# Optimization experiments

Measured on AMD Instinct MI355X. Metric: run time of the kernel, lower is better.

Reference implementation:

```python
import jax, jax.numpy as jnp
import numpy as np

N = 100000
E = 3200000
D = 128


def setup_inputs() -> dict:
    key = jax.random.key(0)
    k1, k2, k3, k4 = jax.random.split(key, 4)
    x = jax.random.normal(k1, (N, D), dtype=jnp.float32)
    edge_index = jax.random.randint(k2, (2, E), 0, N, dtype=jnp.int64)
    W1 = jax.random.normal(k3, (D, 16), dtype=jnp.float32) * (1.0 / np.sqrt(D))
    b1 = jnp.zeros((16,), dtype=jnp.float32)
    W2 = jax.random.normal(k4, (16, 2), dtype=jnp.float32) * (1.0 / np.sqrt(16))
    b2 = jnp.zeros((2,), dtype=jnp.float32)
    return {"x": x, "edge_index": edge_index, "W1": W1, "b1": b1, "W2": W2, "b2": b2}


def _gcn_conv(h, src, dst, norm, W, b):
    # transform first (out_dim <= in_dim), then normalized scatter-add aggregation
    h = h @ W                                   # [N, out]
    msg = h[src] * norm[:, None]                # [E+N, out] gathered messages
    agg = jax.ops.segment_sum(msg, dst, num_segments=N)
    return agg + b


def reference(x, edge_index, W1, b1, W2, b2):
    loops = jnp.arange(N, dtype=edge_index.dtype)
    src = jnp.concatenate([edge_index[0], loops])   # row (message source)
    dst = jnp.concatenate([edge_index[1], loops])   # col (aggregation target)
    # symmetric GCN normalization: deg over dst, norm = d^-1/2[src] * d^-1/2[dst]
    deg = jax.ops.segment_sum(jnp.ones_like(src, dtype=x.dtype), dst, num_segments=N)
    dinv = jnp.where(deg > 0, jax.lax.rsqrt(deg), 0.0)
    norm = dinv[src] * dinv[dst]

    h = _gcn_conv(x, src, dst, norm, W1, b1)
    h = jax.nn.relu(h)
    h = _gcn_conv(h, src, dst, norm, W2, b2)
    return jax.nn.log_softmax(h, axis=1)
```

## Files before the change

### kernel.cpp

```cpp
#include <hip/hip_runtime.h>
#include <hip/hip_fp16.h>
#include <math.h>

#define N_NODES 100000
#define N_EDGES 3200000
#define D_IN    128
#define H1      16

#define PSH     8
#define NPB     200
#define NB      500
#define CAP     9936
#define PBLK    512
#define CHUNK   6250
#define ELS_CAP 13760
#define NLINES  (ELS_CAP / 16)
#define MROWS   64

__device__ __forceinline__ unsigned bkt(int d) {
    return (unsigned)(((unsigned long long)(unsigned)d * 671089ull) >> 27);
}


__global__ __launch_bounds__(512) void k_partition(const int* __restrict__ ei,
                                                   int* __restrict__ cursor,
                                                   unsigned int* __restrict__ eop) {
    __shared__ int h[512];
    __shared__ int loff[512];
    __shared__ int resv[NB];
    __shared__ int wsum[8], wpre[8];
    __shared__ unsigned short owner[NLINES];
    __shared__ unsigned char rank8[CHUNK];
    __shared__ unsigned int els[ELS_CAP];
    int t = threadIdx.x;
    h[t] = 0;
    __syncthreads();
    int c0 = blockIdx.x * CHUNK;
    const int2* s2 = (const int2*)(ei + c0);
    const int2* d2 = (const int2*)(ei + N_EDGES + c0);
    for (int i = t; i < CHUNK / 2; i += 512) {
        int2 dd = d2[i];
        rank8[2 * i]     = (unsigned char)atomicAdd(&h[bkt(dd.x)], 1);
        rank8[2 * i + 1] = (unsigned char)atomicAdd(&h[bkt(dd.y)], 1);
    }
    __syncthreads();
    int cp = (h[t] + 15) & ~15;
    int lane = t & 63, w = t >> 6;
    int v = cp;
#pragma unroll
    for (int o = 1; o < 64; o <<= 1) {
        int u = __shfl_up(v, o);
        if (lane >= o) v += u;
    }
    if (lane == 63) wsum[w] = v;
    __syncthreads();
    if (t < 8) {
        int s = wsum[t];
#pragma unroll
        for (int o = 1; o < 8; o <<= 1) {
            int u = __shfl_up(s, o);
            if (t >= o) s += u;
        }
        wpre[t] = s;
    }
    __syncthreads();
    int inc = v + ((w > 0) ? wpre[w - 1] : 0);
    int totalpad = wpre[7];
    int ex = inc - cp;
    loff[t] = ex;
    if (t < NB && cp) {
        resv[t] = atomicAdd(&cursor[t], cp);
        int l0 = ex >> 4;
        for (int k = 0; k < (cp >> 4); ++k) owner[l0 + k] = (unsigned short)t;
    }
    for (int i = t; i < totalpad; i += 512) els[i] = 0xFFFFFFFFu;
    __syncthreads();
    for (int i = t; i < CHUNK / 2; i += 512) {
        int2 ss = s2[i];
        int2 dd = d2[i];
        unsigned bx = bkt(dd.x), by = bkt(dd.y);
        els[loff[bx] + (int)rank8[2 * i]] =
            ((unsigned)ss.x << PSH) | (unsigned)(dd.x - (int)(bx * NPB));
        els[loff[by] + (int)rank8[2 * i + 1]] =
            ((unsigned)ss.y << PSH) | (unsigned)(dd.y - (int)(by * NPB));
    }
    __syncthreads();
    for (int i = t; i < totalpad; i += 512) {
        int b   = owner[i >> 4];
        int pos = resv[b] + (i - loff[b]);
        if (pos < CAP)
            eop[(size_t)b * CAP + pos] = els[i];
    }
}

__global__ __launch_bounds__(512) void k_build(const int* __restrict__ cursor,
                                               unsigned int* __restrict__ eop,
                                               int* __restrict__ nstart,
                                               int* __restrict__ ndeg,
                                               float* __restrict__ dinv) {
    __shared__ unsigned int els[CAP];
    __shared__ int cnt[256];
    __shared__ int off[256];
    __shared__ int wsum[4], wpre[4];
    int t = threadIdx.x, b = blockIdx.x;
    if (t < 256) cnt[t] = 0;
    __syncthreads();
    int n = cursor[b]; if (n > CAP) n = CAP;
    unsigned int* reg = eop + (size_t)b * CAP;
    for (int i4 = t; i4 < (n >> 2); i4 += 512) {
        uint4 wv = ((const uint4*)reg)[i4];
        unsigned int e0 = wv.x, e1 = wv.y, e2 = wv.z, e3 = wv.w;
        int r;
        if ((int)e0 >= 0) { r = atomicAdd(&cnt[e0 & 0xFF], 1); e0 |= (unsigned)r << 25; }
        if ((int)e1 >= 0) { r = atomicAdd(&cnt[e1 & 0xFF], 1); e1 |= (unsigned)r << 25; }
        if ((int)e2 >= 0) { r = atomicAdd(&cnt[e2 & 0xFF], 1); e2 |= (unsigned)r << 25; }
        if ((int)e3 >= 0) { r = atomicAdd(&cnt[e3 & 0xFF], 1); e3 |= (unsigned)r << 25; }
        ((uint4*)els)[i4] = make_uint4(e0, e1, e2, e3);
    }
    __syncthreads();
    int lane = t & 63, w = t >> 6;
    int v = 0;
    if (t < 256) {
        v = cnt[t];
#pragma unroll
        for (int o = 1; o < 64; o <<= 1) {
            int u = __shfl_up(v, o);
            if (lane >= o) v += u;
        }
        if (lane == 63) wsum[w] = v;
    }
    __syncthreads();
    if (t < 4) {
        int s = wsum[t];
#pragma unroll
        for (int o = 1; o < 4; o <<= 1) {
            int u = __shfl_up(s, o);
            if (t >= o) s += u;
        }
        wpre[t] = s;
    }
    __syncthreads();
    if (t < 256) {
        int val = cnt[t];
        int ex = (v + ((w > 0) ? wpre[w - 1] : 0)) - val;
        off[t] = ex;
        if (t < NPB) {
            int node = b * NPB + t;
            nstart[node] = b * CAP + ex;
            ndeg[node]   = val;
            dinv[node]   = rsqrtf((float)(val + 1));
        }
    }
    __syncthreads();
    for (int i4 = t; i4 < (n >> 2); i4 += 512) {
        uint4 wv = ((const uint4*)els)[i4];
        unsigned int e; unsigned s;
        e = wv.x; s = (e >> PSH) & 0x1FFFFu;
        if (s < N_NODES) reg[off[e & 0xFF] + (int)(e >> 25)] = s;
        e = wv.y; s = (e >> PSH) & 0x1FFFFu;
        if (s < N_NODES) reg[off[e & 0xFF] + (int)(e >> 25)] = s;
        e = wv.z; s = (e >> PSH) & 0x1FFFFu;
        if (s < N_NODES) reg[off[e & 0xFF] + (int)(e >> 25)] = s;
        e = wv.w; s = (e >> PSH) & 0x1FFFFu;
        if (s < N_NODES) reg[off[e & 0xFF] + (int)(e >> 25)] = s;
    }
}

__global__ __launch_bounds__(256) void k_mm1(const float* __restrict__ x,
                                             const float* __restrict__ W1,
                                             const float* __restrict__ dinv,
                                             __half* __restrict__ h1h) {
    __shared__ float sX[MROWS][D_IN + 1];
    int t = threadIdx.x;
    int r0 = blockIdx.x * MROWS;
    for (int i = t; i < MROWS * (D_IN / 4); i += 256) {
        int row = i >> 5, c4 = i & 31;
        int grow = r0 + row;
        float4 v = (grow < N_NODES) ? ((const float4*)x)[(size_t)grow * 32 + c4]
                                    : make_float4(0.f, 0.f, 0.f, 0.f);
        sX[row][c4 * 4 + 0] = v.x; sX[row][c4 * 4 + 1] = v.y;
        sX[row][c4 * 4 + 2] = v.z; sX[row][c4 * 4 + 3] = v.w;
    }
    __syncthreads();
    int lane = t & 63;
    int c0 = __builtin_amdgcn_readfirstlane((t >> 6) * 4);
    float a0 = 0.f, a1 = 0.f, a2 = 0.f, a3 = 0.f;
#pragma unroll 4
    for (int d = 0; d < D_IN; ++d) {
        float xv = sX[lane][d];
        a0 = fmaf(xv, W1[d * 16 + c0 + 0], a0);
        a1 = fmaf(xv, W1[d * 16 + c0 + 1], a1);
        a2 = fmaf(xv, W1[d * 16 + c0 + 2], a2);
        a3 = fmaf(xv, W1[d * 16 + c0 + 3], a3);
    }
    int grow = r0 + lane;
    if (grow < N_NODES) {
        float di = dinv[grow];
        __half2* o = (__half2*)(h1h + (size_t)grow * H1 + c0);
        o[0] = __floats2half2_rn(a0 * di, a1 * di);
        o[1] = __floats2half2_rn(a2 * di, a3 * di);
    }
}

__global__ __launch_bounds__(256) void k_agg1(const unsigned int* __restrict__ eop,
                                              const int* __restrict__ nstart,
                                              const int* __restrict__ ndeg,
                                              const __half* __restrict__ h1h,
                                              const float* __restrict__ dinv,
                                              const float* __restrict__ b1,
                                              const float* __restrict__ W2,
                                              float2* __restrict__ h2f) {
    int t = threadIdx.x;
    int g = t >> 3, l = t & 7;
    int base = (t & 63) & ~7;
    int node = blockIdx.x * 32 + g;
    int e0 = nstart[node], deg = ndeg[node];
    const __half2* H = (const __half2*)h1h;
    float a0 = 0.f, a1 = 0.f, c0 = 0.f, c1 = 0.f;
    int nfull = deg & ~7;
    int j = e0;
    for (; j < e0 + nfull; j += 8) {
        int s = (int)eop[j + l];
#pragma unroll
        for (int k = 0; k < 8; k += 2) {
            int sk0 = __shfl(s, base + k);
            int sk1 = __shfl(s, base + k + 1);
            float2 f0 = __half22float2(H[sk0 * 8 + l]);
            float2 f1 = __half22float2(H[sk1 * 8 + l]);
            a0 += f0.x; a1 += f0.y;
            c0 += f1.x; c1 += f1.y;
        }
    }
    int r = e0 + deg - j;
    if (r) {
        int s = (l < r) ? (int)eop[j + l] : -1;
#pragma unroll
        for (int k = 0; k < 8; ++k) {
            int sk = __shfl(s, base + k);
            int su = (sk >= 0) ? sk : 0;
            float m = (sk >= 0) ? 1.f : 0.f;
            float2 f = __half22float2(H[su * 8 + l]);
            a0 = fmaf(f.x, m, a0); a1 = fmaf(f.y, m, a1);
        }
    }
    float di = dinv[node];
    float2 self = __half22float2(H[node * 8 + l]);
    float s0 = (a0 + c0) + self.x, s1 = (a1 + c1) + self.y;
    float2 bb = ((const float2*)b1)[l];
    float h0 = fmaxf(fmaf(di, s0, bb.x), 0.f);
    float h1v = fmaxf(fmaf(di, s1, bb.y), 0.f);
    float4 wv = ((const float4*)W2)[l];
    float p0 = h0 * wv.x + h1v * wv.z;
    float p1 = h0 * wv.y + h1v * wv.w;
#pragma unroll
    for (int off = 1; off < 8; off <<= 1) {
        p0 += __shfl_xor(p0, off);
        p1 += __shfl_xor(p1, off);
    }
    if (l == 0) h2f[node] = make_float2(p0 * di, p1 * di);
}

__global__ __launch_bounds__(256) void k_agg2(const unsigned int* __restrict__ eop,
                                              const int* __restrict__ nstart,
                                              const int* __restrict__ ndeg,
                                              const float2* __restrict__ h2f,
                                              const float* __restrict__ dinv,
                                              const float* __restrict__ b2,
                                              float* __restrict__ out) {
    int tg = blockIdx.x * 256 + threadIdx.x;
    int node = tg >> 2, l = tg & 3;
    if (node >= N_NODES) return;
    int e0 = nstart[node], e1 = e0 + ndeg[node];
    float ax = 0.f, ay = 0.f;
    for (int j = e0 + l; j < e1; j += 4) {
        float2 m = h2f[eop[j]];
        ax += m.x; ay += m.y;
    }
    ax += __shfl_xor(ax, 1); ay += __shfl_xor(ay, 1);
    ax += __shfl_xor(ax, 2); ay += __shfl_xor(ay, 2);
    if (l == 0) {
        float di = dinv[node];
        float2 self = h2f[node];
        float a0 = fmaf(di, ax + self.x, b2[0]);
        float a1 = fmaf(di, ay + self.y, b2[1]);
        float m  = fmaxf(a0, a1);
        float lg = logf(expf(a0 - m) + expf(a1 - m));
        out[2 * node]     = a0 - m - lg;
        out[2 * node + 1] = a1 - m - lg;
    }
}

extern "C" void kernel_launch(void* const* d_in, const int* in_sizes, int n_in,
                              void* d_out, int out_size, void* d_ws, size_t ws_size,
                              hipStream_t stream) {
    const float* x  = (const float*)d_in[0];
    const int*   ei = (const int*)d_in[1];
    const float* W1 = (const float*)d_in[2];
    const float* b1 = (const float*)d_in[3];
    const float* W2 = (const float*)d_in[4];
    const float* b2 = (const float*)d_in[5];
    float* out = (float*)d_out;

    int*          cursor = (int*)d_ws;
    int*          nstart = cursor + 512;
    int*          ndeg   = nstart + 100352;
    float*        dinv   = (float*)(ndeg + 100352);
    __half*       h1h    = (__half*)(dinv + 100352);
    float2*       h2f    = (float2*)(h1h + (size_t)100352 * H1);
    unsigned int* eop    = (unsigned int*)(h2f + 100352);

    hipMemsetAsync(cursor, 0, 512 * sizeof(int), stream);
    k_partition<<<PBLK, 512, 0, stream>>>(ei, cursor, eop);
    k_build    <<<NB,   512, 0, stream>>>(cursor, eop, nstart, ndeg, dinv);
    k_mm1      <<<(N_NODES + MROWS - 1) / MROWS, 256, 0, stream>>>(x, W1, dinv, h1h);
    k_agg1     <<<N_NODES / 32, 256, 0, stream>>>(eop, nstart, ndeg, h1h, dinv, b1, W2, h2f);
    k_agg2     <<<(N_NODES * 4 + 255) / 256, 256, 0, stream>>>(eop, nstart, ndeg, h2f, dinv, b2, out);
}
```

Before: 204.0 us.

## Scatter partitioned edges directly to global, pad cursors, widen agg2 lanes

The partition kernel no longer stages edges in a large shared-memory buffer with prefix sums and an owner table. It now writes each edge straight to its global bucket slot and pads each reservation with sentinel values. Per-bucket cursors are spaced 32 ints apart so the atomics on them do not contend within a cache line. The second aggregation uses 8 lanes per node instead of 4. Dropping the large LDS buffer should raise occupancy, at the cost of scattered, uncoalesced global writes.

Measured after the change: 221.7 us. 8.7% more time.

```diff
diff --git a/kernel.cpp b/kernel.cpp
--- a/kernel.cpp
+++ b/kernel.cpp
@@ -13,8 +13,7 @@
 #define CAP     9936
 #define PBLK    512
 #define CHUNK   6250
-#define ELS_CAP 13760
-#define NLINES  (ELS_CAP / 16)
+#define CSTRIDE 32
 #define MROWS   64
 
 __device__ __forceinline__ unsigned bkt(int d) {
@@ -26,12 +25,8 @@
                                                    int* __restrict__ cursor,
                                                    unsigned int* __restrict__ eop) {
     __shared__ int h[512];
-    __shared__ int loff[512];
     __shared__ int resv[NB];
-    __shared__ int wsum[8], wpre[8];
-    __shared__ unsigned short owner[NLINES];
     __shared__ unsigned char rank8[CHUNK];
-    __shared__ unsigned int els[ELS_CAP];
     int t = threadIdx.x;
     h[t] = 0;
     __syncthreads();
@@ -44,52 +39,30 @@
         rank8[2 * i + 1] = (unsigned char)atomicAdd(&h[bkt(dd.y)], 1);
     }
     __syncthreads();
-    int cp = (h[t] + 15) & ~15;
-    int lane = t & 63, w = t >> 6;
-    int v = cp;
-#pragma unroll
-    for (int o = 1; o < 64; o <<= 1) {
-        int u = __shfl_up(v, o);
-        if (lane >= o) v += u;
-    }
-    if (lane == 63) wsum[w] = v;
-    __syncthreads();
-    if (t < 8) {
-        int s = wsum[t];
-#pragma unroll
-        for (int o = 1; o < 8; o <<= 1) {
-            int u = __shfl_up(s, o);
-            if (t >= o) s += u;
-        }
-        wpre[t] = s;
-    }
-    __syncthreads();
-    int inc = v + ((w > 0) ? wpre[w - 1] : 0);
-    int totalpad = wpre[7];
-    int ex = inc - cp;
-    loff[t] = ex;
-    if (t < NB && cp) {
-        resv[t] = atomicAdd(&cursor[t], cp);
-        int l0 = ex >> 4;
-        for (int k = 0; k < (cp >> 4); ++k) owner[l0 + k] = (unsigned short)t;
-    }
-    for (int i = t; i < totalpad; i += 512) els[i] = 0xFFFFFFFFu;
+    if (t < NB) {
+        int cnt = h[t];
+        int cp  = (cnt + 15) & ~15;
+        int rv  = cp ? atomicAdd(&cursor[t * CSTRIDE], cp) : 0;
+        resv[t] = rv;
+        unsigned int* regb = eop + (size_t)t * CAP;
+        for (int i = cnt; i < cp; ++i) {
+            int pos = rv + i;
+            if (pos < CAP) regb[pos] = 0xFFFFFFFFu;
+        }
+    }
     __syncthreads();
     for (int i = t; i < CHUNK / 2; i += 512) {
         int2 ss = s2[i];
         int2 dd = d2[i];
         unsigned bx = bkt(dd.x), by = bkt(dd.y);
-        els[loff[bx] + (int)rank8[2 * i]] =
-            ((unsigned)ss.x << PSH) | (unsigned)(dd.x - (int)(bx * NPB));
-        els[loff[by] + (int)rank8[2 * i + 1]] =
-            ((unsigned)ss.y << PSH) | (unsigned)(dd.y - (int)(by * NPB));
-    }
-    __syncthreads();
-    for (int i = t; i < totalpad; i += 512) {
-        int b   = owner[i >> 4];
-        int pos = resv[b] + (i - loff[b]);
-        if (pos < CAP)
-            eop[(size_t)b * CAP + pos] = els[i];
+        int px = resv[bx] + (int)rank8[2 * i];
+        int py = resv[by] + (int)rank8[2 * i + 1];
+        if (px < CAP)
+            eop[(size_t)bx * CAP + px] =
+                ((unsigned)ss.x << PSH) | (unsigned)(dd.x - (int)(bx * NPB));
+        if (py < CAP)
+            eop[(size_t)by * CAP + py] =
+                ((unsigned)ss.y << PSH) | (unsigned)(dd.y - (int)(by * NPB));
     }
 }
 
@@ -105,7 +78,7 @@
     int t = threadIdx.x, b = blockIdx.x;
     if (t < 256) cnt[t] = 0;
     __syncthreads();
-    int n = cursor[b]; if (n > CAP) n = CAP;
+    int n = cursor[b * CSTRIDE]; if (n > CAP) n = CAP;
     unsigned int* reg = eop + (size_t)b * CAP;
     for (int i4 = t; i4 < (n >> 2); i4 += 512) {
         uint4 wv = ((const uint4*)reg)[i4];
@@ -268,16 +241,16 @@
                                               const float* __restrict__ b2,
                                               float* __restrict__ out) {
     int tg = blockIdx.x * 256 + threadIdx.x;
-    int node = tg >> 2, l = tg & 3;
-    if (node >= N_NODES) return;
+    int node = tg >> 3, l = tg & 7;
     int e0 = nstart[node], e1 = e0 + ndeg[node];
     float ax = 0.f, ay = 0.f;
-    for (int j = e0 + l; j < e1; j += 4) {
+    for (int j = e0 + l; j < e1; j += 8) {
         float2 m = h2f[eop[j]];
         ax += m.x; ay += m.y;
     }
     ax += __shfl_xor(ax, 1); ay += __shfl_xor(ay, 1);
     ax += __shfl_xor(ax, 2); ay += __shfl_xor(ay, 2);
+    ax += __shfl_xor(ax, 4); ay += __shfl_xor(ay, 4);
     if (l == 0) {
         float di = dinv[node];
         float2 self = h2f[node];
@@ -302,17 +275,18 @@
     float* out = (float*)d_out;
 
     int*          cursor = (int*)d_ws;
-    int*          nstart = cursor + 512;
+    int*          nstart = cursor + 16384;
     int*          ndeg   = nstart + 100352;
     float*        dinv   = (float*)(ndeg + 100352);
     __half*       h1h    = (__half*)(dinv + 100352);
     float2*       h2f    = (float2*)(h1h + (size_t)100352 * H1);
     unsigned int* eop    = (unsigned int*)(h2f + 100352);
 
-    hipMemsetAsync(cursor, 0, 512 * sizeof(int), stream);
+    hipMemsetAsync(cursor, 0, 16384 * sizeof(int), stream);
+
     k_partition<<<PBLK, 512, 0, stream>>>(ei, cursor, eop);
     k_build    <<<NB,   512, 0, stream>>>(cursor, eop, nstart, ndeg, dinv);
     k_mm1      <<<(N_NODES + MROWS - 1) / MROWS, 256, 0, stream>>>(x, W1, dinv, h1h);
     k_agg1     <<<N_NODES / 32, 256, 0, stream>>>(eop, nstart, ndeg, h1h, dinv, b1, W2, h2f);
-    k_agg2     <<<(N_NODES * 4 + 255) / 256, 256, 0, stream>>>(eop, nstart, ndeg, h2f, dinv, b2, out);
-}
+    k_agg2     <<<N_NODES / 32, 256, 0, stream>>>(eop, nstart, ndeg, h2f, dinv, b2, out);
+}
```
